# Performance work log

Hardware: AMD Instinct MI355X
Metric: run time of the kernel (lower is better)

Reference implementation:

```python
import jax, jax.numpy as jnp
import numpy as np

N_FEAT = 1024
NEG_BIG = -1e30  # finite stand-in for -inf to avoid NaNs on fully-masked rows


def setup_inputs() -> dict:
    key = jax.random.key(0)
    k1, k2, k3 = jax.random.split(key, 3)
    T, C = 4096, 1024
    x = jax.random.normal(k1, (T, C), dtype=jnp.float32)
    W = jax.random.normal(k2, (C, 3 * N_FEAT), dtype=jnp.float32) * 0.02
    b = jax.random.normal(k3, (3 * N_FEAT,), dtype=jnp.float32) * 0.02
    return {"x": x, "W": W, "b": b, "n_padd": 256}


def reference(x, W, b, n_padd):
    T, C = x.shape
    qkv = x @ W + b  # [T, 3*N_FEAT]
    q, k, v = jnp.split(qkv, 3, axis=1)  # each [T, N_FEAT]
    att = (q @ k.T) * (1.0 / jnp.sqrt(jnp.float32(N_FEAT)))  # [T, T]
    idx = jnp.arange(T)
    causal = idx[None, :] <= idx[:, None]
    data = (idx[None, :] >= n_padd) & (idx[:, None] >= n_padd)
    mask = causal & data
    att = jnp.where(mask, att, NEG_BIG)
    p = jax.nn.softmax(att, axis=-1)  # fully-masked rows -> uniform, zeroed below
    y = p @ v  # [T, N_FEAT]
    # kernel only stores rows >= n_padd; padded rows defined as zero here
    y = jnp.where(idx[:, None] >= n_padd, y, 0.0)
    return y
```

## Files before the change

### kernel.cpp

```cpp
#include <hip/hip_runtime.h>
#include <hip/hip_bf16.h>
#include <stdint.h>
#include <stddef.h>

#define TT 4096
#define CC 1024
#define NFD 1024
#define N3 3072
#define PB0 1152
#define PB2 2176
#define PB3 3200

typedef __bf16 bf16;
typedef __bf16 bf16x8 __attribute__((ext_vector_type(8)));
typedef __bf16 bf16x4 __attribute__((ext_vector_type(4)));
typedef float f32x4 __attribute__((ext_vector_type(4)));

typedef const __attribute__((address_space(1))) unsigned char gl_u8;
typedef __attribute__((address_space(3))) unsigned char lds_u8;

__device__ __forceinline__ void glds16(const void* g, void* l) {
  __builtin_amdgcn_global_load_lds((gl_u8*)g, (lds_u8*)l, 16, 0, 0);
}

__device__ __forceinline__ void stage128x32(const bf16* __restrict__ src, int ld, bf16* lds, int tid) {
  const int lane = tid & 63;
  const int w = tid >> 6;
#pragma unroll
  for (int p = 0; p < 2; ++p) {
    const int lbyte = w * 2048 + p * 1024;
    const int row = (lbyte >> 6) + (lane >> 2);
    const int kel = (lane & 3) << 3;
    glds16(src + row * ld + kel, (char*)lds + lbyte);
  }
}

__device__ __forceinline__ void gemm_core(const bf16* __restrict__ A, const bf16* __restrict__ B,
                                          int lda, int ldb, int ksteps,
                                          bf16* As, bf16* Bs, int tid, f32x4 (&acc)[4][4]) {
  const int lane = tid & 63;
  const int w = tid >> 6;
  const int wm = (w >> 1) * 64;
  const int wn = (w & 1) * 64;
  const int lrow = lane & 15;
  const int lko = (lane >> 4) * 8;
  stage128x32(A, lda, As, tid);
  stage128x32(B, ldb, Bs, tid);
  __syncthreads();
  for (int ks = 0; ks < ksteps; ++ks) {
    const bf16* Ac = As + (ks & 1) * 4096;
    const bf16* Bc = Bs + (ks & 1) * 4096;
    if (ks + 1 < ksteps) {
      stage128x32(A + (ks + 1) * 32, lda, As + ((ks + 1) & 1) * 4096, tid);
      stage128x32(B + (ks + 1) * 32, ldb, Bs + ((ks + 1) & 1) * 4096, tid);
    }
    bf16x8 af[4], bfr[4];
#pragma unroll
    for (int i = 0; i < 4; ++i)
      af[i] = *(const bf16x8*)(Ac + (wm + i * 16 + lrow) * 32 + lko);
#pragma unroll
    for (int i = 0; i < 4; ++i)
      bfr[i] = *(const bf16x8*)(Bc + (wn + i * 16 + lrow) * 32 + lko);
#pragma unroll
    for (int mi = 0; mi < 4; ++mi)
#pragma unroll
      for (int ni = 0; ni < 4; ++ni)
        acc[mi][ni] = __builtin_amdgcn_mfma_f32_16x16x32_bf16(af[mi], bfr[ni], acc[mi][ni], 0, 0, 0);
    __syncthreads();
  }
}

__global__ __launch_bounds__(256) void k_prep(const float* __restrict__ x, bf16* __restrict__ xb,
                                              const float* __restrict__ Wsrc, bf16* __restrict__ WbT,
                                              float* __restrict__ l) {
  __shared__ float Ls[64][65];
  const int tid = threadIdx.x;
  if (blockIdx.x < 2048) {
    int idx = (blockIdx.x * 256 + tid) * 8;
    f32x4 a = *(const f32x4*)(x + idx);
    f32x4 b = *(const f32x4*)(x + idx + 4);
    bf16x8 o;
#pragma unroll
    for (int j = 0; j < 4; ++j) { o[j] = (bf16)a[j]; o[4 + j] = (bf16)b[j]; }
    *(bf16x8*)(xb + idx) = o;
    return;
  }
  if (blockIdx.x == 2048 + 768) {
    f32x4 z = (f32x4){0.f, 0.f, 0.f, 0.f};
#pragma unroll
    for (int qq = 0; qq < 4; ++qq)
      *(f32x4*)(l + (qq * 256 + tid) * 4) = z;
    return;
  }
  const int bid = blockIdx.x - 2048;
  const int n0 = (bid % 48) * 64;
  const int c0 = (bid / 48) * 64;
#pragma unroll
  for (int qq = 0; qq < 4; ++qq) {
    int lin = qq * 1024 + tid * 4;
    int r = lin >> 6, cc = lin & 63;
    f32x4 v = *(const f32x4*)(Wsrc + (size_t)(c0 + r) * N3 + n0 + cc);
#pragma unroll
    for (int j = 0; j < 4; ++j) Ls[r][cc + j] = v[j];
  }
  __syncthreads();
#pragma unroll
  for (int qq = 0; qq < 4; ++qq) {
    int lin = qq * 1024 + tid * 4;
    int nr = lin >> 6, cc = lin & 63;
    bf16x4 o;
#pragma unroll
    for (int j = 0; j < 4; ++j) o[j] = (bf16)Ls[cc + j][nr];
    *(bf16x4*)(WbT + (size_t)(n0 + nr) * CC + c0 + cc) = o;
  }
}

__global__ __launch_bounds__(256, 2) void k_qkv(const bf16* __restrict__ xb, const bf16* __restrict__ wbt,
                                                const float* __restrict__ bias,
                                                bf16* __restrict__ q, bf16* __restrict__ k,
                                                bf16* __restrict__ vT) {
  __shared__ bf16 As[2 * 128 * 32], Bs[2 * 128 * 32];
  const int tid = threadIdx.x;
  const int id = blockIdx.x;
  const int r = id & 7;
  const int s = id >> 3;
  const int it = 4 * r + (s & 3);
  const int jt = s >> 2;
  const int m0 = it * 128;
  const int n0 = jt * 128;
  f32x4 acc[4][4];
#pragma unroll
  for (int i = 0; i < 4; ++i)
#pragma unroll
    for (int j = 0; j < 4; ++j) acc[i][j] = (f32x4){0.f, 0.f, 0.f, 0.f};

  gemm_core(xb + (size_t)m0 * CC, wbt + (size_t)n0 * CC, CC, CC, CC / 32, As, Bs, tid, acc);

  const int lane = tid & 63;
  const int w = tid >> 6;
  const int wm = (w >> 1) * 64, wn = (w & 1) * 64;
  const int seg = n0 >> 10;
#pragma unroll
  for (int mi = 0; mi < 4; ++mi) {
    const int tB = m0 + wm + mi * 16 + ((lane >> 4) << 2);
#pragma unroll
    for (int ni = 0; ni < 4; ++ni) {
      const int n = n0 + wn + ni * 16 + (lane & 15);
      const float bb = bias[n];
      f32x4 a = acc[mi][ni];
      if (seg == 2) {
        bf16x4 pv;
#pragma unroll
        for (int r2 = 0; r2 < 4; ++r2) pv[r2] = (bf16)(a[r2] + bb);
        *(bf16x4*)(vT + (size_t)(n - 2048) * TT + tB) = pv;
      } else {
        bf16* dst = (seg == 0) ? q : k;
        const int nl = n & 1023;
#pragma unroll
        for (int r2 = 0; r2 < 4; ++r2) dst[(size_t)(tB + r2) * NFD + nl] = (bf16)(a[r2] + bb);
      }
    }
  }
}

__global__ __launch_bounds__(256, 2) void k_scores(const bf16* __restrict__ q, const bf16* __restrict__ kk,
                                                   bf16* __restrict__ P, float* __restrict__ l,
                                                   const int* __restrict__ npadd_p) {
  const int id = blockIdx.x;
  const int lin = (id & 7) * 66 + (id >> 3);
  int band, rem;
  if (lin < 228)      { band = 0; rem = lin; }
  else if (lin < 392) { band = 1; rem = lin - 228; }
  else if (lin < 492) { band = 2; rem = lin - 392; }
  else                { band = 3; rem = lin - 492; }
  int it, jt;
  if (rem < 28) {
    int itp = (int)((sqrtf(8.0f * (float)rem + 1.0f) - 1.0f) * 0.5f);
    while ((itp + 1) * (itp + 2) / 2 <= rem) ++itp;
    while (itp * (itp + 1) / 2 > rem) --itp;
    it = band * 8 + itp;
    jt = band * 8 + (rem - itp * (itp + 1) / 2);
  } else {
    const int rem2 = rem - 28;
    it = band * 8 + 7 + (rem2 >> 3);
    jt = band * 8 + (rem2 & 7);
  }
  const int np = *npadd_p;
  const int jt0 = np >> 7;
  if (jt < jt0) return;

  __shared__ bf16 As[2 * 128 * 32], Bs[2 * 128 * 32];
  const int tid = threadIdx.x;
  f32x4 acc[4][4];
#pragma unroll
  for (int i = 0; i < 4; ++i)
#pragma unroll
    for (int j = 0; j < 4; ++j) acc[i][j] = (f32x4){0.f, 0.f, 0.f, 0.f};

  gemm_core(q + (size_t)it * 128 * CC, kk + (size_t)jt * 128 * CC, CC, CC, CC / 32, As, Bs, tid, acc);

  const int lane = tid & 63;
  const int w = tid >> 6;
  const int wm = (w >> 1) * 64, wn = (w & 1) * 64;
  const float scale = 0.03125f;
#pragma unroll
  for (int mi = 0; mi < 4; ++mi) {
    const int iB = it * 128 + wm + mi * 16 + ((lane >> 4) << 2);
    float rs[4] = {0.f, 0.f, 0.f, 0.f};
#pragma unroll
    for (int ni = 0; ni < 4; ++ni) {
      const int j = jt * 128 + wn + ni * 16 + (lane & 15);
      f32x4 a = acc[mi][ni];
#pragma unroll
      for (int r = 0; r < 4; ++r) {
        const int i = iB + r;
        float p = 0.f;
        if (j <= i && j >= np && i >= np) p = __expf(a[r] * scale);
        const bf16 pb = (bf16)p;
        P[(size_t)i * TT + j] = pb;
        rs[r] += (float)pb;
      }
    }
#pragma unroll
    for (int r = 0; r < 4; ++r) {
      float v = rs[r];
      v += __shfl_xor(v, 1);
      v += __shfl_xor(v, 2);
      v += __shfl_xor(v, 4);
      v += __shfl_xor(v, 8);
      if ((lane & 15) == 0) atomicAdd(&l[iB + r], v);
    }
  }
}

__global__ __launch_bounds__(256, 2) void k_pvc(const bf16* __restrict__ P, const bf16* __restrict__ vT,
                                                bf16* __restrict__ part0, bf16* __restrict__ part1,
                                                bf16* __restrict__ part2, bf16* __restrict__ part3,
                                                const float* __restrict__ l, float* __restrict__ y,
                                                const int* __restrict__ npadd_p) {
  const int id = blockIdx.x;
  const int kgrp = id >> 3;
  const int d0 = (kgrp & 7) * 128;
  const int p = (id & 7) + 8 * (kgrp >> 3);
  const int it = p >> 2;
  const int c = p & 3;
  const int np = *npadd_p;
  const int jt0 = np >> 7;
  const int lo = (c == 0) ? 0 : (c == 1 ? 9 : (c == 2 ? 17 : 25));
  const int hi = (c == 0) ? 9 : (c == 1 ? 17 : (c == 2 ? 25 : 32));
  const int jlo = max(lo, jt0);
  const int jhi = min(hi, it + 1);
  if (jlo >= jhi) return;

  __shared__ bf16 As[2 * 128 * 32], Bs[2 * 128 * 32];
  const int tid = threadIdx.x;
  f32x4 acc[4][4];
#pragma unroll
  for (int i = 0; i < 4; ++i)
#pragma unroll
    for (int j = 0; j < 4; ++j) acc[i][j] = (f32x4){0.f, 0.f, 0.f, 0.f};

  gemm_core(P + (size_t)it * 128 * TT + (size_t)jlo * 128,
            vT + (size_t)d0 * TT + (size_t)jlo * 128,
            TT, TT, (jhi - jlo) * 4, As, Bs, tid, acc);

  const int lane = tid & 63;
  const int w = tid >> 6;
  const int wm = (w >> 1) * 64, wn = (w & 1) * 64;
  const bool sole = (jlo == jt0) && (jhi == it + 1);
  if (sole) {
#pragma unroll
    for (int mi = 0; mi < 4; ++mi) {
      const int iB = it * 128 + wm + mi * 16 + ((lane >> 4) << 2);
      float inv4[4];
#pragma unroll
      for (int r = 0; r < 4; ++r) {
        const int i = iB + r;
        inv4[r] = (i >= np) ? (1.0f / l[i]) : 0.0f;
      }
#pragma unroll
      for (int ni = 0; ni < 4; ++ni) {
        const int d = d0 + wn + ni * 16 + (lane & 15);
        f32x4 a = acc[mi][ni];
#pragma unroll
        for (int r = 0; r < 4; ++r)
          y[(size_t)(iB + r) * NFD + d] = a[r] * inv4[r];
      }
    }
  } else {
    bf16* __restrict__ part = (c == 0) ? part0 : (c == 1 ? part1 : (c == 2 ? part2 : part3));
    const int base = (c == 3) ? (PB3 * NFD) : ((c == 2) ? (PB2 * NFD) : (PB0 * NFD));
#pragma unroll
    for (int mi = 0; mi < 4; ++mi) {
      const int iB = it * 128 + wm + mi * 16 + ((lane >> 4) << 2);
#pragma unroll
      for (int ni = 0; ni < 4; ++ni) {
        const int d = d0 + wn + ni * 16 + (lane & 15);
        f32x4 a = acc[mi][ni];
#pragma unroll
        for (int r = 0; r < 4; ++r)
          part[(size_t)(iB + r) * NFD + d - base] = (bf16)a[r];
      }
    }
  }
}

__global__ __launch_bounds__(256) void k_norm(const bf16* __restrict__ part0, const bf16* __restrict__ part1,
                                              const bf16* __restrict__ part2, const bf16* __restrict__ part3,
                                              const float* __restrict__ l, float* __restrict__ y,
                                              const int* __restrict__ npadd_p) {
  const int idx = (blockIdx.x * 256 + threadIdx.x) * 8;
  const int i = idx >> 10;
  const int np = *npadd_p;
  if (i < np) {
    f32x4 z = (f32x4){0.f, 0.f, 0.f, 0.f};
    *(f32x4*)(y + idx) = z;
    *(f32x4*)(y + idx + 4) = z;
    return;
  }
  const int jt0 = np >> 7;
  const int it = i >> 7;
  const int ip1 = it + 1;
  const bool a0 = (max(0, jt0)  < min(9, ip1));
  const bool a1 = (max(9, jt0)  < min(17, ip1));
  const bool a2 = (max(17, jt0) < min(25, ip1));
  const bool a3 = (max(25, jt0) < min(32, ip1));
  const int cnt = (int)a0 + (int)a1 + (int)a2 + (int)a3;
  if (cnt <= 1) return;
  float s[8] = {0.f, 0.f, 0.f, 0.f, 0.f, 0.f, 0.f, 0.f};
  if (a0) {
    bf16x8 a = *(const bf16x8*)(part0 + idx - PB0 * NFD);
#pragma unroll
    for (int j = 0; j < 8; ++j) s[j] += (float)a[j];
  }
  if (a1) {
    bf16x8 a = *(const bf16x8*)(part1 + idx - PB0 * NFD);
#pragma unroll
    for (int j = 0; j < 8; ++j) s[j] += (float)a[j];
  }
  if (a2) {
    bf16x8 a = *(const bf16x8*)(part2 + idx - PB2 * NFD);
#pragma unroll
    for (int j = 0; j < 8; ++j) s[j] += (float)a[j];
  }
  if (a3) {
    bf16x8 a = *(const bf16x8*)(part3 + idx - PB3 * NFD);
#pragma unroll
    for (int j = 0; j < 8; ++j) s[j] += (float)a[j];
  }
  const float inv = 1.0f / l[i];
  f32x4 o0, o1;
#pragma unroll
  for (int j = 0; j < 4; ++j) { o0[j] = s[j] * inv; o1[j] = s[4 + j] * inv; }
  *(f32x4*)(y + idx) = o0;
  *(f32x4*)(y + idx + 4) = o1;
}

extern "C" void kernel_launch(void* const* d_in, const int* in_sizes, int n_in,
                              void* d_out, int out_size, void* d_ws, size_t ws_size,
                              hipStream_t stream) {
  const float* x = (const float*)d_in[0];
  const float* W = (const float*)d_in[1];
  const float* b = (const float*)d_in[2];
  const int* npadd = (const int*)d_in[3];
  float* y = (float*)d_out;

  char* ws = (char*)d_ws;
  const size_t MB = 1u << 20;
  bf16* q  = (bf16*)(ws + 0 * MB);
  bf16* kk = (bf16*)(ws + 8 * MB);
  bf16* part0 = (bf16*)(ws + 0 * MB);
  bf16* part1 = (bf16*)(ws + (size_t)(TT - PB0) * NFD * 2);
  bf16* part2 = (bf16*)(ws + (size_t)2 * (TT - PB0) * NFD * 2);
  bf16* vT = (bf16*)(ws + 16 * MB);
  float* l = (float*)(ws + 24 * MB);
  bf16* P  = (bf16*)(ws + 24 * MB + 65536);
  bf16* xb = P;
  bf16* WbT = (bf16*)((char*)P + 8 * MB);
  bf16* part3 = (bf16*)(ws + 60 * MB);

  k_prep<<<dim3(2048 + 768 + 1), 256, 0, stream>>>(x, xb, W, WbT, l);
  k_qkv<<<dim3(768), 256, 0, stream>>>(xb, WbT, b, q, kk, vT);
  k_scores<<<dim3(528), 256, 0, stream>>>(q, kk, P, l, npadd);
  k_pvc<<<dim3(1024), 256, 0, stream>>>(P, vT, part0, part1, part2, part3, l, y, npadd);
  k_norm<<<dim3((TT * NFD) / (256 * 8)), 256, 0, stream>>>(part0, part1, part2, part3, l, y, npadd);
}
```

Before: 117.0 us.

## Fuse x fp32-to-bf16 conversion into QKV GEMM via swizzled fp32 LDS staging

```diff
diff --git a/kernel.cpp b/kernel.cpp
--- a/kernel.cpp
+++ b/kernel.cpp
@@ -33,6 +33,23 @@
     const int kel = (lane & 3) << 3;
     glds16(src + row * ld + kel, (char*)lds + lbyte);
   }
+}
+
+__device__ __forceinline__ void stage128x32f(const float* __restrict__ src, int ld, float* lds, int tid) {
+  const int lane = tid & 63;
+  const int w = tid >> 6;
+#pragma unroll
+  for (int p = 0; p < 4; ++p) {
+    const int lbyte = w * 4096 + p * 1024;
+    const int row = (lbyte >> 7) + (lane >> 3);
+    const int ch = lane & 7;
+    const int col = ((ch ^ (row & 7)) << 2);
+    glds16(src + (size_t)row * ld + col, (char*)lds + lbyte);
+  }
+}
+
+__device__ __forceinline__ f32x4 ldsA(const float* As, int row, int c) {
+  return *(const f32x4*)((const char*)As + row * 128 + ((c ^ (row & 7)) << 4));
 }
 
 __device__ __forceinline__ void gemm_core(const bf16* __restrict__ A, const bf16* __restrict__ B,
@@ -70,29 +87,59 @@
   }
 }
 
-__global__ __launch_bounds__(256) void k_prep(const float* __restrict__ x, bf16* __restrict__ xb,
-                                              const float* __restrict__ Wsrc, bf16* __restrict__ WbT,
+__device__ __forceinline__ void gemm_core_f32A(const float* __restrict__ A, const bf16* __restrict__ B,
+                                               int lda, int ldb, int ksteps,
+                                               float* As, bf16* Bs, int tid, f32x4 (&acc)[4][4]) {
+  const int lane = tid & 63;
+  const int w = tid >> 6;
+  const int wm = (w >> 1) * 64;
+  const int wn = (w & 1) * 64;
+  const int lrow = lane & 15;
+  const int lko = (lane >> 4) * 8;
+  const int c0 = lko >> 2;
+  stage128x32f(A, lda, As, tid);
+  stage128x32(B, ldb, Bs, tid);
+  __syncthreads();
+  for (int ks = 0; ks < ksteps; ++ks) {
+    const float* Ac = As + (ks & 1) * 4096;
+    const bf16* Bc = Bs + (ks & 1) * 4096;
+    if (ks + 1 < ksteps) {
+      stage128x32f(A + (ks + 1) * 32, lda, As + ((ks + 1) & 1) * 4096, tid);
+      stage128x32(B + (ks + 1) * 32, ldb, Bs + ((ks + 1) & 1) * 4096, tid);
+    }
+    bf16x8 af[4], bfr[4];
+#pragma unroll
+    for (int i = 0; i < 4; ++i) {
+      const int row = wm + i * 16 + lrow;
+      f32x4 lo = ldsA(Ac, row, c0);
+      f32x4 hi = ldsA(Ac, row, c0 + 1);
+#pragma unroll
+      for (int j = 0; j < 4; ++j) { af[i][j] = (bf16)lo[j]; af[i][4 + j] = (bf16)hi[j]; }
+    }
+#pragma unroll
+    for (int i = 0; i < 4; ++i)
+      bfr[i] = *(const bf16x8*)(Bc + (wn + i * 16 + lrow) * 32 + lko);
+#pragma unroll
+    for (int mi = 0; mi < 4; ++mi)
+#pragma unroll
+      for (int ni = 0; ni < 4; ++ni)
+        acc[mi][ni] = __builtin_amdgcn_mfma_f32_16x16x32_bf16(af[mi], bfr[ni], acc[mi][ni], 0, 0, 0);
+    __syncthreads();
+  }
+}
+
+__global__ __launch_bounds__(256) void k_prep(const float* __restrict__ Wsrc, bf16* __restrict__ WbT,
                                               float* __restrict__ l) {
   __shared__ float Ls[64][65];
   const int tid = threadIdx.x;
-  if (blockIdx.x < 2048) {
-    int idx = (blockIdx.x * 256 + tid) * 8;
-    f32x4 a = *(const f32x4*)(x + idx);
-    f32x4 b = *(const f32x4*)(x + idx + 4);
-    bf16x8 o;
-#pragma unroll
-    for (int j = 0; j < 4; ++j) { o[j] = (bf16)a[j]; o[4 + j] = (bf16)b[j]; }
-    *(bf16x8*)(xb + idx) = o;
-    return;
-  }
-  if (blockIdx.x == 2048 + 768) {
+  if (blockIdx.x == 768) {
     f32x4 z = (f32x4){0.f, 0.f, 0.f, 0.f};
 #pragma unroll
     for (int qq = 0; qq < 4; ++qq)
       *(f32x4*)(l + (qq * 256 + tid) * 4) = z;
     return;
   }
-  const int bid = blockIdx.x - 2048;
+  const int bid = blockIdx.x;
   const int n0 = (bid % 48) * 64;
   const int c0 = (bid / 48) * 64;
 #pragma unroll
@@ -115,11 +162,12 @@
   }
 }
 
-__global__ __launch_bounds__(256, 2) void k_qkv(const bf16* __restrict__ xb, const bf16* __restrict__ wbt,
+__global__ __launch_bounds__(256, 2) void k_qkv(const float* __restrict__ x, const bf16* __restrict__ wbt,
                                                 const float* __restrict__ bias,
                                                 bf16* __restrict__ q, bf16* __restrict__ k,
                                                 bf16* __restrict__ vT) {
-  __shared__ bf16 As[2 * 128 * 32], Bs[2 * 128 * 32];
+  __shared__ float Asf[2 * 128 * 32];
+  __shared__ bf16 Bs[2 * 128 * 32];
   const int tid = threadIdx.x;
   const int id = blockIdx.x;
   const int r = id & 7;
@@ -134,7 +182,7 @@
 #pragma unroll
     for (int j = 0; j < 4; ++j) acc[i][j] = (f32x4){0.f, 0.f, 0.f, 0.f};
 
-  gemm_core(xb + (size_t)m0 * CC, wbt + (size_t)n0 * CC, CC, CC, CC / 32, As, Bs, tid, acc);
+  gemm_core_f32A(x + (size_t)m0 * CC, wbt + (size_t)n0 * CC, CC, CC, CC / 32, Asf, Bs, tid, acc);
 
   const int lane = tid & 63;
   const int w = tid >> 6;
@@ -375,12 +423,11 @@
   bf16* vT = (bf16*)(ws + 16 * MB);
   float* l = (float*)(ws + 24 * MB);
   bf16* P  = (bf16*)(ws + 24 * MB + 65536);
-  bf16* xb = P;
-  bf16* WbT = (bf16*)((char*)P + 8 * MB);
+  bf16* WbT = (bf16*)P;
   bf16* part3 = (bf16*)(ws + 60 * MB);
 
-  k_prep<<<dim3(2048 + 768 + 1), 256, 0, stream>>>(x, xb, W, WbT, l);
-  k_qkv<<<dim3(768), 256, 0, stream>>>(xb, WbT, b, q, kk, vT);
+  k_prep<<<dim3(768 + 1), 256, 0, stream>>>(W, WbT, l);
+  k_qkv<<<dim3(768), 256, 0, stream>>>(x, WbT, b, q, kk, vT);
   k_scores<<<dim3(528), 256, 0, stream>>>(q, kk, P, l, npadd);
   k_pvc<<<dim3(1024), 256, 0, stream>>>(P, vT, part0, part1, part2, part3, l, y, npadd);
   k_norm<<<dim3((TT * NFD) / (256 * 8)), 256, 0, stream>>>(part0, part1, part2, part3, l, y, npadd);
```

Measured after the change: 126.8 us. 1.08x slower.

## Fuse split-K reduction into PV kernel via atomic tickets, drop k_norm launch

Applied to the files above, without the earlier changes.

```diff
diff --git a/kernel.cpp b/kernel.cpp
--- a/kernel.cpp
+++ b/kernel.cpp
@@ -72,7 +72,7 @@
 
 __global__ __launch_bounds__(256) void k_prep(const float* __restrict__ x, bf16* __restrict__ xb,
                                               const float* __restrict__ Wsrc, bf16* __restrict__ WbT,
-                                              float* __restrict__ l) {
+                                              float* __restrict__ l, int* __restrict__ tickets) {
   __shared__ float Ls[64][65];
   const int tid = threadIdx.x;
   if (blockIdx.x < 2048) {
@@ -90,6 +90,7 @@
 #pragma unroll
     for (int qq = 0; qq < 4; ++qq)
       *(f32x4*)(l + (qq * 256 + tid) * 4) = z;
+    tickets[tid] = 0;
     return;
   }
   const int bid = blockIdx.x - 2048;
@@ -237,6 +238,7 @@
                                                 bf16* __restrict__ part0, bf16* __restrict__ part1,
                                                 bf16* __restrict__ part2, bf16* __restrict__ part3,
                                                 const float* __restrict__ l, float* __restrict__ y,
+                                                int* __restrict__ tickets,
                                                 const int* __restrict__ npadd_p) {
   const int id = blockIdx.x;
   const int kgrp = id >> 3;
@@ -250,10 +252,19 @@
   const int hi = (c == 0) ? 9 : (c == 1 ? 17 : (c == 2 ? 25 : 32));
   const int jlo = max(lo, jt0);
   const int jhi = min(hi, it + 1);
-  if (jlo >= jhi) return;
+  const int tid = threadIdx.x;
+  if (jlo >= jhi) {
+    if (c == 0 && it + 1 <= jt0) {
+      const int rr = tid >> 1, cb = (tid & 1) * 64;
+      float* yrow = y + (size_t)(it * 128 + rr) * NFD + d0 + cb;
+      f32x4 z = (f32x4){0.f, 0.f, 0.f, 0.f};
+#pragma unroll
+      for (int ch = 0; ch < 16; ++ch) *(f32x4*)(yrow + ch * 4) = z;
+    }
+    return;
+  }
 
   __shared__ bf16 As[2 * 128 * 32], Bs[2 * 128 * 32];
-  const int tid = threadIdx.x;
   f32x4 acc[4][4];
 #pragma unroll
   for (int i = 0; i < 4; ++i)
@@ -287,73 +298,68 @@
           y[(size_t)(iB + r) * NFD + d] = a[r] * inv4[r];
       }
     }
-  } else {
-    bf16* __restrict__ part = (c == 0) ? part0 : (c == 1 ? part1 : (c == 2 ? part2 : part3));
-    const int base = (c == 3) ? (PB3 * NFD) : ((c == 2) ? (PB2 * NFD) : (PB0 * NFD));
-#pragma unroll
-    for (int mi = 0; mi < 4; ++mi) {
-      const int iB = it * 128 + wm + mi * 16 + ((lane >> 4) << 2);
-#pragma unroll
-      for (int ni = 0; ni < 4; ++ni) {
-        const int d = d0 + wn + ni * 16 + (lane & 15);
-        f32x4 a = acc[mi][ni];
-#pragma unroll
-        for (int r = 0; r < 4; ++r)
-          part[(size_t)(iB + r) * NFD + d - base] = (bf16)a[r];
-      }
-    }
-  }
-}
-
-__global__ __launch_bounds__(256) void k_norm(const bf16* __restrict__ part0, const bf16* __restrict__ part1,
-                                              const bf16* __restrict__ part2, const bf16* __restrict__ part3,
-                                              const float* __restrict__ l, float* __restrict__ y,
-                                              const int* __restrict__ npadd_p) {
-  const int idx = (blockIdx.x * 256 + threadIdx.x) * 8;
-  const int i = idx >> 10;
-  const int np = *npadd_p;
-  if (i < np) {
-    f32x4 z = (f32x4){0.f, 0.f, 0.f, 0.f};
-    *(f32x4*)(y + idx) = z;
-    *(f32x4*)(y + idx + 4) = z;
     return;
   }
-  const int jt0 = np >> 7;
-  const int it = i >> 7;
+  bf16* __restrict__ part = (c == 0) ? part0 : (c == 1 ? part1 : (c == 2 ? part2 : part3));
+  const int base = (c == 3) ? (PB3 * NFD) : ((c == 2) ? (PB2 * NFD) : (PB0 * NFD));
+#pragma unroll
+  for (int mi = 0; mi < 4; ++mi) {
+    const int iB = it * 128 + wm + mi * 16 + ((lane >> 4) << 2);
+#pragma unroll
+    for (int ni = 0; ni < 4; ++ni) {
+      const int d = d0 + wn + ni * 16 + (lane & 15);
+      f32x4 a = acc[mi][ni];
+#pragma unroll
+      for (int r = 0; r < 4; ++r)
+        part[(size_t)(iB + r) * NFD + d - base] = (bf16)a[r];
+    }
+  }
+  __threadfence();
+  __shared__ int s_old;
+  if (tid == 0) s_old = atomicAdd(&tickets[it * 8 + (d0 >> 7)], 1);
+  __syncthreads();
   const int ip1 = it + 1;
   const bool a0 = (max(0, jt0)  < min(9, ip1));
   const bool a1 = (max(9, jt0)  < min(17, ip1));
   const bool a2 = (max(17, jt0) < min(25, ip1));
   const bool a3 = (max(25, jt0) < min(32, ip1));
   const int cnt = (int)a0 + (int)a1 + (int)a2 + (int)a3;
-  if (cnt <= 1) return;
-  float s[8] = {0.f, 0.f, 0.f, 0.f, 0.f, 0.f, 0.f, 0.f};
-  if (a0) {
-    bf16x8 a = *(const bf16x8*)(part0 + idx - PB0 * NFD);
-#pragma unroll
-    for (int j = 0; j < 8; ++j) s[j] += (float)a[j];
-  }
-  if (a1) {
-    bf16x8 a = *(const bf16x8*)(part1 + idx - PB0 * NFD);
-#pragma unroll
-    for (int j = 0; j < 8; ++j) s[j] += (float)a[j];
-  }
-  if (a2) {
-    bf16x8 a = *(const bf16x8*)(part2 + idx - PB2 * NFD);
-#pragma unroll
-    for (int j = 0; j < 8; ++j) s[j] += (float)a[j];
-  }
-  if (a3) {
-    bf16x8 a = *(const bf16x8*)(part3 + idx - PB3 * NFD);
-#pragma unroll
-    for (int j = 0; j < 8; ++j) s[j] += (float)a[j];
-  }
-  const float inv = 1.0f / l[i];
-  f32x4 o0, o1;
-#pragma unroll
-  for (int j = 0; j < 4; ++j) { o0[j] = s[j] * inv; o1[j] = s[4 + j] * inv; }
-  *(f32x4*)(y + idx) = o0;
-  *(f32x4*)(y + idx + 4) = o1;
+  if (s_old != cnt - 1) return;
+  __threadfence();
+  const int rr = tid >> 1, cb = (tid & 1) * 64;
+  const int g = it * 128 + rr;
+  const float inv = (g >= np) ? (1.0f / l[g]) : 0.0f;
+  const size_t rowoff = (size_t)g * NFD + d0 + cb;
+#pragma unroll
+  for (int ch = 0; ch < 8; ++ch) {
+    const size_t off = rowoff + ch * 8;
+    float s[8] = {0.f, 0.f, 0.f, 0.f, 0.f, 0.f, 0.f, 0.f};
+    if (a0) {
+      bf16x8 a = *(const bf16x8*)(part0 + off - (size_t)PB0 * NFD);
+#pragma unroll
+      for (int j = 0; j < 8; ++j) s[j] += (float)a[j];
+    }
+    if (a1) {
+      bf16x8 a = *(const bf16x8*)(part1 + off - (size_t)PB0 * NFD);
+#pragma unroll
+      for (int j = 0; j < 8; ++j) s[j] += (float)a[j];
+    }
+    if (a2) {
+      bf16x8 a = *(const bf16x8*)(part2 + off - (size_t)PB2 * NFD);
+#pragma unroll
+      for (int j = 0; j < 8; ++j) s[j] += (float)a[j];
+    }
+    if (a3) {
+      bf16x8 a = *(const bf16x8*)(part3 + off - (size_t)PB3 * NFD);
+#pragma unroll
+      for (int j = 0; j < 8; ++j) s[j] += (float)a[j];
+    }
+    f32x4 o0, o1;
+#pragma unroll
+    for (int j = 0; j < 4; ++j) { o0[j] = s[j] * inv; o1[j] = s[4 + j] * inv; }
+    *(f32x4*)(y + off) = o0;
+    *(f32x4*)(y + off + 4) = o1;
+  }
 }
 
 extern "C" void kernel_launch(void* const* d_in, const int* in_sizes, int n_in,
@@ -374,14 +380,14 @@
   bf16* part2 = (bf16*)(ws + (size_t)2 * (TT - PB0) * NFD * 2);
   bf16* vT = (bf16*)(ws + 16 * MB);
   float* l = (float*)(ws + 24 * MB);
+  int* tickets = (int*)(ws + 24 * MB + 16384);
   bf16* P  = (bf16*)(ws + 24 * MB + 65536);
   bf16* xb = P;
   bf16* WbT = (bf16*)((char*)P + 8 * MB);
   bf16* part3 = (bf16*)(ws + 60 * MB);
 
-  k_prep<<<dim3(2048 + 768 + 1), 256, 0, stream>>>(x, xb, W, WbT, l);
+  k_prep<<<dim3(2048 + 768 + 1), 256, 0, stream>>>(x, xb, W, WbT, l, tickets);
   k_qkv<<<dim3(768), 256, 0, stream>>>(xb, WbT, b, q, kk, vT);
   k_scores<<<dim3(528), 256, 0, stream>>>(q, kk, P, l, npadd);
-  k_pvc<<<dim3(1024), 256, 0, stream>>>(P, vT, part0, part1, part2, part3, l, y, npadd);
-  k_norm<<<dim3((TT * NFD) / (256 * 8)), 256, 0, stream>>>(part0, part1, part2, part3, l, y, npadd);
-}
+  k_pvc<<<dim3(1024), 256, 0, stream>>>(P, vT, part0, part1, part2, part3, l, y, tickets, npadd);
+}
```

New measurement: 415.4 us. 3.55x slower.
